# Optimization experiments

Hardware: AMD Instinct MI355X
Metric: run time of the kernel (lower is better)

The kernel has to match this reference:

```python
import jax, jax.numpy as jnp
import numpy as np

NUM_EXPERTS = 4  # matches init_kwargs

def setup_inputs() -> dict:
    key = jax.random.key(0)
    ks = jax.random.split(key, 6)
    B, T, D = 4, 4096, 1024
    H = 4 * D
    x = jax.random.normal(ks[0], (B, T, D), dtype=jnp.float32)
    token_mask = jax.random.randint(ks[1], (B, T), 0, NUM_EXPERTS, dtype=jnp.int32)
    s1 = 1.0 / np.sqrt(D)
    s2 = 1.0 / np.sqrt(H)
    W1 = jax.random.normal(ks[2], (H, D), dtype=jnp.float32) * s1
    b1 = jax.random.normal(ks[3], (H,), dtype=jnp.float32) * s1
    W2 = jax.random.normal(ks[4], (D, H), dtype=jnp.float32) * s2
    b2 = jax.random.normal(ks[5], (D,), dtype=jnp.float32) * s2
    return {"x": x, "token_mask": token_mask, "W1": W1, "b1": b1, "W2": W2, "b2": b2}

def reference(x, token_mask, W1, b1, W2, b2):
    # Nested MoE FFN: expert m uses leading D//2^(E-1-m) input dims and
    # leading H//2^(E-1-m) hidden dims; top expert (m=E-1) is the full MLP.
    D = x.shape[-1]
    H = W1.shape[0]
    factor = 2 ** (NUM_EXPERTS - 1 - token_mask)          # [B,T] int
    d_in = D // factor                                     # [B,T]
    d_hid = H // factor                                    # [B,T]
    mask_in = (jnp.arange(D) < d_in[..., None]).astype(x.dtype)    # [B,T,D]
    mask_hid = (jnp.arange(H) < d_hid[..., None]).astype(x.dtype)  # [B,T,H]
    # Expand: slice input dims, project, keep only nested hidden slice (bias included only there)
    h = (jnp.einsum('btd,hd->bth', x * mask_in, W1) + b1) * mask_hid
    h = jax.nn.gelu(h, approximate=False)  # gelu(0)=0 preserves nested zeros
    # Contract: zeros outside the nested hidden slice contribute nothing; full output + bias
    out = jnp.einsum('bth,dh->btd', h, W2) + b2
    return out
```

## Files before the change

kernel.cpp:

```cpp
#include <hip/hip_runtime.h>
#include <cstdint>
#include <math.h>

typedef __attribute__((ext_vector_type(8))) __bf16 bf16x8;
typedef __attribute__((ext_vector_type(4))) float f32x4;
typedef unsigned short ushort_t;

__device__ __forceinline__ ushort_t f2bf(float f) {
    uint32_t u = __float_as_uint(f);
    u += 0x7fff + ((u >> 16) & 1);
    return (ushort_t)(u >> 16);
}

__device__ __forceinline__ float gelu_fast(float x) {
    float u = x * (0.7978845608f + 0.0356774081f * x * x);
    float e = __expf(2.0f * u);
    float th = 1.0f - 2.0f / (e + 1.0f);
    return 0.5f * x * (1.0f + th);
}

__device__ __forceinline__ float gelu_exact(float v) {
    return 0.5f * v * (1.0f + erff(v * 0.70710678118654752440f));
}

__global__ void histo_convw_kernel(const int* __restrict__ tm, int* __restrict__ cnt,
                                   int nchunks,
                                   const float* __restrict__ s1, const float* __restrict__ s2,
                                   ushort_t* __restrict__ d1, ushort_t* __restrict__ d2,
                                   int n4) {
    if (blockIdx.x < (unsigned)nchunks) {
        __shared__ int h[4];
        if (threadIdx.x < 4) h[threadIdx.x] = 0;
        __syncthreads();
        int e = tm[blockIdx.x * 256 + threadIdx.x];
        atomicAdd(&h[e], 1);
        __syncthreads();
        if (threadIdx.x < 4) cnt[blockIdx.x * 4 + threadIdx.x] = h[threadIdx.x];
    } else {
        const int stride = (gridDim.x - nchunks) * 256;
        for (int i = (blockIdx.x - nchunks) * 256 + threadIdx.x; i < 2 * n4; i += stride) {
            const float* src; ushort_t* dst; int k;
            if (i < n4) { src = s1; dst = d1; k = i; }
            else        { src = s2; dst = d2; k = i - n4; }
            const float4 v = ((const float4*)src)[k];
            ushort4 o;
            o.x = f2bf(v.x); o.y = f2bf(v.y); o.z = f2bf(v.z); o.w = f2bf(v.w);
            ((ushort4*)dst)[k] = o;
        }
    }
}

__global__ void meta_kernel(int* __restrict__ meta, int* __restrict__ cnt,
                            int* __restrict__ sidx, int nchunks, int D, int H) {
    __shared__ int tot[4];
    __shared__ int soff_s[4];
    const int t = threadIdx.x;
    const int e = t >> 6;
    const int c0 = t & 63;
    int carry = 0;
    for (int base = 0; base < nchunks; base += 64) {
        int c = base + c0;
        int v = (c < nchunks) ? cnt[c * 4 + e] : 0;
        int s = v;
#pragma unroll
        for (int d = 1; d < 64; d <<= 1) {
            int y = __shfl_up(s, d);
            if (c0 >= d) s += y;
        }
        if (c < nchunks) cnt[c * 4 + e] = s - v + carry;
        carry += __shfl(s, 63);
    }
    if (c0 == 0) tot[e] = carry;
    __syncthreads();
    if (t == 0) {
        int off = 0, xoff = 0, hoff = 0;
        for (int ee = 0; ee < 4; ee++) {
            int c = tot[ee];
            int ac = (c + 127) & ~127;
            meta[ee] = c; meta[4 + ee] = off; meta[8 + ee] = ac; meta[12 + ee] = ac >> 7;
            meta[16 + ee] = xoff; meta[20 + ee] = hoff;
            soff_s[ee] = off;
            off += ac; xoff += ac * (D >> (3 - ee)); hoff += ac * (H >> (3 - ee));
        }
        meta[28] = off;
        int a = 0, b = 0;
        for (int k = 0; k < 4; k++) {
            int ee = 3 - k;
            meta[24 + k] = a; a += meta[12 + ee] * ((H >> (3 - ee)) >> 7);
            meta[32 + k] = b; b += meta[12 + ee] * (D >> 7);
        }
        meta[29] = a; meta[36] = b;
    }
    __syncthreads();
    for (int base = 0; base < 64 * ((nchunks + 63) / 64); base += 64) {
        int c = base + c0;
        if (c < nchunks) cnt[c * 4 + e] += soff_s[e];
    }
    for (int ee = 0; ee < 4; ee++) {
        int s0 = soff_s[ee] + tot[ee];
        int n = meta[8 + ee] - tot[ee];
        for (int i = t; i < n; i += 256) sidx[s0 + i] = -1;
    }
}

__global__ void place_kernel(const int* __restrict__ tm, const int* __restrict__ cofs,
                             int* __restrict__ sidx) {
    __shared__ unsigned char se[256];
    const int c = blockIdx.x;
    const int t = threadIdx.x;
    const int tok = c * 256 + t;
    const int e = tm[tok];
    se[t] = (unsigned char)e;
    __syncthreads();
    int rank = 0;
    for (int i = 0; i < t; i++) rank += (se[i] == (unsigned char)e);
    sidx[cofs[c * 4 + e] + rank] = tok;
}

__global__ void convert_x_sorted(const float* __restrict__ x,
                                 const int* __restrict__ meta,
                                 const int* __restrict__ sidx,
                                 ushort_t* __restrict__ xb, int D) {
    const int rows = meta[28];
    for (int p = blockIdx.x; p < rows; p += gridDim.x) {
        const int e = (p >= meta[5]) + (p >= meta[6]) + (p >= meta[7]);
        const int off = meta[4 + e];
        const int din = D >> (3 - e);
        const int tok = sidx[p];
        ushort_t* dst = xb + (size_t)meta[16 + e] + (size_t)(p - off) * din;
        const int c = threadIdx.x * 4;
        if (c < din) {
            if (tok < 0) {
                *(ushort4*)(dst + c) = ushort4{0, 0, 0, 0};
            } else {
                const float4 v = *(const float4*)(x + (size_t)tok * D + c);
                ushort4 o;
                o.x = f2bf(v.x); o.y = f2bf(v.y); o.z = f2bf(v.z); o.w = f2bf(v.w);
                *(ushort4*)(dst + c) = o;
            }
        }
    }
}

__device__ __forceinline__ void stage4(const ushort_t* Ag, const ushort_t* Bg,
                                       int lda, int ldb,
                                       char* AsB, char* BsB, int ldsoff) {
    __builtin_amdgcn_global_load_lds(
        (__attribute__((address_space(1))) void*)(uintptr_t)Ag,
        (__attribute__((address_space(3))) void*)(AsB + ldsoff), 16, 0, 0);
    __builtin_amdgcn_global_load_lds(
        (__attribute__((address_space(1))) void*)(uintptr_t)(Ag + (size_t)64 * lda),
        (__attribute__((address_space(3))) void*)(AsB + 4096 + ldsoff), 16, 0, 0);
    __builtin_amdgcn_global_load_lds(
        (__attribute__((address_space(1))) void*)(uintptr_t)Bg,
        (__attribute__((address_space(3))) void*)(BsB + ldsoff), 16, 0, 0);
    __builtin_amdgcn_global_load_lds(
        (__attribute__((address_space(1))) void*)(uintptr_t)(Bg + (size_t)64 * ldb),
        (__attribute__((address_space(3))) void*)(BsB + 4096 + ldsoff), 16, 0, 0);
}

template <int EPI>
__global__ void gemm_sorted(const ushort_t* __restrict__ Abuf,
                            const ushort_t* __restrict__ Bw,
                            const float* __restrict__ bias,
                            const int* __restrict__ meta,
                            const int* __restrict__ sidx,
                            ushort_t* __restrict__ hb,
                            float* __restrict__ out,
                            int D, int H) {
    __shared__ ushort_t As[3][128 * 32];
    __shared__ ushort_t Bs[3][128 * 32];

    const int t    = threadIdx.x;
    const int wave = t >> 6;
    const int lane = t & 63;
    const int quad = lane >> 4;
    const int l16  = lane & 15;
    const int wm   = wave & 1;
    const int wn   = wave >> 1;
    const int srow = t >> 2;
    const int scol = (t & 3) * 8;
    const int ldsoff = wave * 64 * 16;

    const int* st = meta + (EPI == 0 ? 24 : 32);
    const int  T  = meta[EPI == 0 ? 29 : 36];

    for (int idx = blockIdx.x; idx < T; idx += gridDim.x) {
        const int k3 = (idx >= st[1]) + (idx >= st[2]) + (idx >= st[3]);
        const int e = 3 - k3;
        const int local = idx - st[k3];
        const int mtiles = meta[12 + e];
        const int mt = local % mtiles;
        const int nt = local / mtiles;

        const int K   = (EPI == 0) ? (D >> (3 - e)) : (H >> (3 - e));
        const int Ne  = (EPI == 0) ? (H >> (3 - e)) : D;
        const int lda = K;
        const int ldb = (EPI == 0) ? D : H;
        const int nb  = nt * 128;
        const ushort_t* A = Abuf + (size_t)((EPI == 0) ? meta[16 + e] : meta[20 + e]);

        const ushort_t* Ag = A + (size_t)(mt * 128 + srow) * lda + scol;
        const ushort_t* Bg = Bw + (size_t)(nb + srow) * ldb + scol;

        const int nsteps = K >> 5;

        f32x4 acc[4][4] = {};

        stage4(Ag,      Bg,      lda, ldb, (char*)As[0], (char*)Bs[0], ldsoff);
        stage4(Ag + 32, Bg + 32, lda, ldb, (char*)As[1], (char*)Bs[1], ldsoff);
        stage4(Ag + 64, Bg + 64, lda, ldb, (char*)As[2], (char*)Bs[2], ldsoff);

        int cur = 0;
        for (int s = 0; s < nsteps; ++s) {
            const int rem = nsteps - s;
            if (rem > 2)       { asm volatile("s_waitcnt vmcnt(8)" ::: "memory"); }
            else if (rem == 2) { asm volatile("s_waitcnt vmcnt(4)" ::: "memory"); }
            else               { asm volatile("s_waitcnt vmcnt(0)" ::: "memory"); }
            __builtin_amdgcn_s_barrier();
            asm volatile("" ::: "memory");

            bf16x8 af[4], bfr[4];
#pragma unroll
            for (int i = 0; i < 4; i++) {
                af[i]  = *(const bf16x8*)(As[cur] + (wm * 64 + i * 16 + l16) * 32 + quad * 8);
                bfr[i] = *(const bf16x8*)(Bs[cur] + (wn * 64 + i * 16 + l16) * 32 + quad * 8);
            }
            asm volatile("s_waitcnt lgkmcnt(0)" ::: "memory");
            __builtin_amdgcn_s_barrier();
            asm volatile("" ::: "memory");

            if (s + 3 < nsteps)
                stage4(Ag + (size_t)(s + 3) * 32, Bg + (size_t)(s + 3) * 32,
                       lda, ldb, (char*)As[cur], (char*)Bs[cur], ldsoff);

#pragma unroll
            for (int i = 0; i < 4; i++)
#pragma unroll
                for (int j = 0; j < 4; j++)
                    acc[i][j] = __builtin_amdgcn_mfma_f32_16x16x32_bf16(af[i], bfr[j], acc[i][j], 0, 0, 0);

            cur = (cur == 2) ? 0 : cur + 1;
        }

        const int colbase = nb + wn * 64 + l16;
        float bv[4];
#pragma unroll
        for (int j = 0; j < 4; j++) bv[j] = bias[colbase + j * 16];

#pragma unroll
        for (int i = 0; i < 4; i++) {
#pragma unroll
            for (int r = 0; r < 4; r++) {
                const int lrow = mt * 128 + wm * 64 + i * 16 + quad * 4 + r;
                if (EPI == 0) {
                    ushort_t* dst = hb + (size_t)meta[20 + e] + (size_t)lrow * Ne;
#pragma unroll
                    for (int j = 0; j < 4; j++)
                        dst[colbase + j * 16] = f2bf(gelu_fast(acc[i][j][r] + bv[j]));
                } else {
                    const int tok = sidx[meta[4 + e] + lrow];
                    if (tok >= 0) {
                        float* dst = out + (size_t)tok * D;
#pragma unroll
                        for (int j = 0; j < 4; j++)
                            dst[colbase + j * 16] = acc[i][j][r] + bv[j];
                    }
                }
            }
        }
    }
}

__global__ void naive_kernel(const float* __restrict__ x, const int* __restrict__ tm,
                             const float* __restrict__ W1, const float* __restrict__ b1,
                             const float* __restrict__ W2, const float* __restrict__ b2,
                             float* __restrict__ out, int D, int Hdim) {
    const int t = blockIdx.x;
    const int m = tm[t];
    const int din = D >> (3 - m);
    const int dh = Hdim >> (3 - m);
    extern __shared__ float sm[];
    float* xs = sm;
    float* hs = sm + D;
    for (int i = threadIdx.x; i < din; i += blockDim.x) xs[i] = x[(size_t)t * D + i];
    __syncthreads();
    for (int h = threadIdx.x; h < dh; h += blockDim.x) {
        const float* w = W1 + (size_t)h * D;
        float a = b1[h];
        for (int d = 0; d < din; d++) a += xs[d] * w[d];
        hs[h] = gelu_exact(a);
    }
    __syncthreads();
    for (int d = threadIdx.x; d < D; d += blockDim.x) {
        const float* w = W2 + (size_t)d * Hdim;
        float a = b2[d];
        for (int h = 0; h < dh; h++) a += hs[h] * w[h];
        out[(size_t)t * D + d] = a;
    }
}

extern "C" void kernel_launch(void* const* d_in, const int* in_sizes, int n_in,
                              void* d_out, int out_size, void* d_ws, size_t ws_size,
                              hipStream_t stream) {
    const float* x  = (const float*)d_in[0];
    const int* tm   = (const int*)d_in[1];
    const float* W1 = (const float*)d_in[2];
    const float* b1 = (const float*)d_in[3];
    const float* W2 = (const float*)d_in[4];
    const float* b2 = (const float*)d_in[5];
    float* out = (float*)d_out;

    const int M    = in_sizes[1];
    const int Hdim = in_sizes[3];
    const int D    = in_sizes[0] / M;

    const int Mpad = M + 512;
    const int nchunks = M / 256;
    const size_t meta_sz = 256;
    const size_t cnt_sz  = ((size_t)nchunks * 4 * 4 + 255) & ~(size_t)255;
    const size_t sidx_sz = ((size_t)Mpad * 4 + 255) & ~(size_t)255;
    const size_t xb_sz   = (size_t)Mpad * D * 2;
    const size_t w1_sz   = (size_t)Hdim * D * 2;
    const size_t w2_sz   = (size_t)D * Hdim * 2;
    const size_t hb_sz   = (size_t)Mpad * Hdim * 2;
    const size_t need_sorted = meta_sz + cnt_sz + sidx_sz + xb_sz + w1_sz + w2_sz + hb_sz;

    const bool shape_ok = (M % 256 == 0) && (D % 128 == 0) && (Hdim % 128 == 0) &&
                          (D >= 1024) && (D <= 1024) && (Hdim >= 4096);

    if (shape_ok && ws_size >= need_sorted) {
        char* p = (char*)d_ws;
        int* meta     = (int*)p;        p += meta_sz;
        int* cnt      = (int*)p;        p += cnt_sz;
        int* sidx     = (int*)p;        p += sidx_sz;
        ushort_t* xb  = (ushort_t*)p;   p += xb_sz;
        ushort_t* w1b = (ushort_t*)p;   p += w1_sz;
        ushort_t* w2b = (ushort_t*)p;   p += w2_sz;
        ushort_t* hb  = (ushort_t*)p;

        const int n4w = Hdim * D / 4;
        histo_convw_kernel<<<nchunks + 2048, 256, 0, stream>>>(tm, cnt, nchunks,
                                                               W1, W2, w1b, w2b, n4w);
        meta_kernel<<<1, 256, 0, stream>>>(meta, cnt, sidx, nchunks, D, Hdim);
        place_kernel<<<nchunks, 256, 0, stream>>>(tm, cnt, sidx);
        convert_x_sorted<<<2048, 256, 0, stream>>>(x, meta, sidx, xb, D);

        gemm_sorted<0><<<2048, 256, 0, stream>>>(xb, w1b, b1, meta, sidx, hb, nullptr, D, Hdim);
        gemm_sorted<1><<<2048, 256, 0, stream>>>(hb, w2b, b2, meta, sidx, nullptr, out, D, Hdim);
        return;
    }

    const size_t shmem = (size_t)(D + Hdim) * sizeof(float);
    naive_kernel<<<M, 256, shmem, stream>>>(x, tm, W1, b1, W2, b2, out, D, Hdim);
}
```

Before: 330.3 us.

## Use atomic tile scheduler and split-K within block for second GEMM

Both GEMMs now pull tile indices from a global atomic counter rather than using a static grid-stride loop. Launches are sized to a fixed number of persistent blocks. The second GEMM runs 512 threads per block as two 256-thread groups, each handling half of K with its own LDS triple buffer, then reduces through shared memory before the scattered output write. The aim is better load balance across the largest-first expert tiles and more parallelism for the long-K, few-tile second GEMM, at the cost of atomics, extra barriers, a shared-memory reduction and lower occupancy from 96KB of LDS.

```diff
diff --git a/kernel.cpp b/kernel.cpp
--- a/kernel.cpp
+++ b/kernel.cpp
@@ -90,6 +90,8 @@
             meta[32 + k] = b; b += meta[12 + ee] * (D >> 7);
         }
         meta[29] = a; meta[36] = b;
+        meta[48] = 0;
+        meta[49] = 0;
     }
     __syncthreads();
     for (int base = 0; base < 64 * ((nchunks + 63) / 64); base += 64) {
@@ -159,17 +161,16 @@
         (__attribute__((address_space(3))) void*)(BsB + 4096 + ldsoff), 16, 0, 0);
 }
 
-template <int EPI>
-__global__ void gemm_sorted(const ushort_t* __restrict__ Abuf,
-                            const ushort_t* __restrict__ Bw,
-                            const float* __restrict__ bias,
-                            const int* __restrict__ meta,
-                            const int* __restrict__ sidx,
-                            ushort_t* __restrict__ hb,
-                            float* __restrict__ out,
-                            int D, int H) {
+__global__ void gemm1_kernel(const ushort_t* __restrict__ Abuf,
+                             const ushort_t* __restrict__ Bw,
+                             const float* __restrict__ bias,
+                             const int* meta,
+                             ushort_t* __restrict__ hb,
+                             int* tctr,
+                             int D, int H) {
     __shared__ ushort_t As[3][128 * 32];
     __shared__ ushort_t Bs[3][128 * 32];
+    __shared__ int s_next;
 
     const int t    = threadIdx.x;
     const int wave = t >> 6;
@@ -182,10 +183,15 @@
     const int scol = (t & 3) * 8;
     const int ldsoff = wave * 64 * 16;
 
-    const int* st = meta + (EPI == 0 ? 24 : 32);
-    const int  T  = meta[EPI == 0 ? 29 : 36];
-
-    for (int idx = blockIdx.x; idx < T; idx += gridDim.x) {
+    const int* st = meta + 24;
+    const int  T  = meta[29];
+
+    while (true) {
+        if (t == 0) s_next = atomicAdd(tctr, 1);
+        __syncthreads();
+        const int idx = s_next;
+        if (idx >= T) break;
+
         const int k3 = (idx >= st[1]) + (idx >= st[2]) + (idx >= st[3]);
         const int e = 3 - k3;
         const int local = idx - st[k3];
@@ -193,12 +199,12 @@
         const int mt = local % mtiles;
         const int nt = local / mtiles;
 
-        const int K   = (EPI == 0) ? (D >> (3 - e)) : (H >> (3 - e));
-        const int Ne  = (EPI == 0) ? (H >> (3 - e)) : D;
+        const int K   = D >> (3 - e);
+        const int Ne  = H >> (3 - e);
         const int lda = K;
-        const int ldb = (EPI == 0) ? D : H;
+        const int ldb = D;
         const int nb  = nt * 128;
-        const ushort_t* A = Abuf + (size_t)((EPI == 0) ? meta[16 + e] : meta[20 + e]);
+        const ushort_t* A = Abuf + (size_t)meta[16 + e];
 
         const ushort_t* Ag = A + (size_t)(mt * 128 + srow) * lda + scol;
         const ushort_t* Bg = Bw + (size_t)(nb + srow) * ldb + scol;
@@ -253,22 +259,153 @@
 #pragma unroll
             for (int r = 0; r < 4; r++) {
                 const int lrow = mt * 128 + wm * 64 + i * 16 + quad * 4 + r;
-                if (EPI == 0) {
-                    ushort_t* dst = hb + (size_t)meta[20 + e] + (size_t)lrow * Ne;
+                ushort_t* dst = hb + (size_t)meta[20 + e] + (size_t)lrow * Ne;
+#pragma unroll
+                for (int j = 0; j < 4; j++)
+                    dst[colbase + j * 16] = f2bf(gelu_fast(acc[i][j][r] + bv[j]));
+            }
+        }
+        __syncthreads();
+    }
+}
+
+__global__ __launch_bounds__(512)
+void gemm2_kernel(const ushort_t* __restrict__ Abuf,
+                  const ushort_t* __restrict__ Bw,
+                  const float* __restrict__ bias,
+                  const int* meta,
+                  const int* __restrict__ sidx,
+                  float* __restrict__ out,
+                  int* tctr,
+                  int D, int H) {
+    __shared__ char smem[98304];
+    __shared__ int s_next;
+
+    const int t    = threadIdx.x;
+    const int g    = t >> 8;
+    const int tl   = t & 255;
+    const int wiv  = tl >> 6;
+    const int lane = t & 63;
+    const int quad = lane >> 4;
+    const int l16  = lane & 15;
+    const int wm   = wiv & 1;
+    const int wn   = wiv >> 1;
+    const int srow = tl >> 2;
+    const int scol = (tl & 3) * 8;
+    const int ldsoff = wiv * 64 * 16;
+
+    const int* st = meta + 32;
+    const int  T  = meta[36];
+
+    while (true) {
+        if (t == 0) s_next = atomicAdd(tctr, 1);
+        __syncthreads();
+        const int idx = s_next;
+        if (idx >= T) break;
+
+        const int k3 = (idx >= st[1]) + (idx >= st[2]) + (idx >= st[3]);
+        const int e = 3 - k3;
+        const int local = idx - st[k3];
+        const int mtiles = meta[12 + e];
+        const int mt = local % mtiles;
+        const int nt = local / mtiles;
+
+        const int Kfull = H >> (3 - e);
+        const int Kh    = Kfull >> 1;
+        const int lda = Kfull;
+        const int ldb = H;
+        const int nb  = nt * 128;
+        const ushort_t* A = Abuf + (size_t)meta[20 + e];
+
+        const ushort_t* Ag = A + (size_t)(mt * 128 + srow) * lda + scol + (size_t)g * Kh;
+        const ushort_t* Bg = Bw + (size_t)(nb + srow) * ldb + scol + (size_t)g * Kh;
+
+        const int nsteps = Kh >> 5;
+
+        char* buf0 = smem + (size_t)(g * 3 + 0) * 16384;
+        char* buf1 = smem + (size_t)(g * 3 + 1) * 16384;
+        char* buf2 = smem + (size_t)(g * 3 + 2) * 16384;
+
+        f32x4 acc[4][4] = {};
+
+        stage4(Ag,      Bg,      lda, ldb, buf0, buf0 + 8192, ldsoff);
+        stage4(Ag + 32, Bg + 32, lda, ldb, buf1, buf1 + 8192, ldsoff);
+        stage4(Ag + 64, Bg + 64, lda, ldb, buf2, buf2 + 8192, ldsoff);
+
+        int cur = 0;
+        for (int s = 0; s < nsteps; ++s) {
+            const int rem = nsteps - s;
+            if (rem > 2)       { asm volatile("s_waitcnt vmcnt(8)" ::: "memory"); }
+            else if (rem == 2) { asm volatile("s_waitcnt vmcnt(4)" ::: "memory"); }
+            else               { asm volatile("s_waitcnt vmcnt(0)" ::: "memory"); }
+            __builtin_amdgcn_s_barrier();
+            asm volatile("" ::: "memory");
+
+            char* bc = smem + (size_t)(g * 3 + cur) * 16384;
+            const ushort_t* Asc = (const ushort_t*)bc;
+            const ushort_t* Bsc = (const ushort_t*)(bc + 8192);
+
+            bf16x8 af[4], bfr[4];
+#pragma unroll
+            for (int i = 0; i < 4; i++) {
+                af[i]  = *(const bf16x8*)(Asc + (wm * 64 + i * 16 + l16) * 32 + quad * 8);
+                bfr[i] = *(const bf16x8*)(Bsc + (wn * 64 + i * 16 + l16) * 32 + quad * 8);
+            }
+            asm volatile("s_waitcnt lgkmcnt(0)" ::: "memory");
+            __builtin_amdgcn_s_barrier();
+            asm volatile("" ::: "memory");
+
+            if (s + 3 < nsteps)
+                stage4(Ag + (size_t)(s + 3) * 32, Bg + (size_t)(s + 3) * 32,
+                       lda, ldb, bc, bc + 8192, ldsoff);
+
+#pragma unroll
+            for (int i = 0; i < 4; i++)
+#pragma unroll
+                for (int j = 0; j < 4; j++)
+                    acc[i][j] = __builtin_amdgcn_mfma_f32_16x16x32_bf16(af[i], bfr[j], acc[i][j], 0, 0, 0);
+
+            cur = (cur == 2) ? 0 : cur + 1;
+        }
+
+        float* red = (float*)smem;
+        __syncthreads();
+        if (g == 1) {
+#pragma unroll
+            for (int i = 0; i < 4; i++)
+#pragma unroll
+                for (int r = 0; r < 4; r++) {
+                    const int lrl = wm * 64 + i * 16 + quad * 4 + r;
 #pragma unroll
                     for (int j = 0; j < 4; j++)
-                        dst[colbase + j * 16] = f2bf(gelu_fast(acc[i][j][r] + bv[j]));
-                } else {
+                        red[lrl * 128 + wn * 64 + j * 16 + l16] = acc[i][j][r];
+                }
+        }
+        __syncthreads();
+        if (g == 0) {
+            const int colbase = nb + wn * 64 + l16;
+            float bv[4];
+#pragma unroll
+            for (int j = 0; j < 4; j++) bv[j] = bias[colbase + j * 16];
+
+#pragma unroll
+            for (int i = 0; i < 4; i++) {
+#pragma unroll
+                for (int r = 0; r < 4; r++) {
+                    const int lrl  = wm * 64 + i * 16 + quad * 4 + r;
+                    const int lrow = mt * 128 + lrl;
                     const int tok = sidx[meta[4 + e] + lrow];
                     if (tok >= 0) {
                         float* dst = out + (size_t)tok * D;
 #pragma unroll
                         for (int j = 0; j < 4; j++)
-                            dst[colbase + j * 16] = acc[i][j][r] + bv[j];
+                            dst[colbase + j * 16] =
+                                acc[i][j][r] + red[lrl * 128 + wn * 64 + j * 16 + l16] + bv[j];
                     }
                 }
             }
         }
+        __syncthreads();
     }
 }
 
@@ -346,8 +483,8 @@
         place_kernel<<<nchunks, 256, 0, stream>>>(tm, cnt, sidx);
         convert_x_sorted<<<2048, 256, 0, stream>>>(x, meta, sidx, xb, D);
 
-        gemm_sorted<0><<<2048, 256, 0, stream>>>(xb, w1b, b1, meta, sidx, hb, nullptr, D, Hdim);
-        gemm_sorted<1><<<2048, 256, 0, stream>>>(hb, w2b, b2, meta, sidx, nullptr, out, D, Hdim);
+        gemm1_kernel<<<768, 256, 0, stream>>>(xb, w1b, b1, meta, hb, meta + 48, D, Hdim);
+        gemm2_kernel<<<256, 512, 0, stream>>>(hb, w2b, b2, meta, sidx, out, meta + 49, D, Hdim);
         return;
     }
 
```

Result: slower. 384.1 us (+16.3%).

## Assign GEMM tiles per XCD for L2 locality and use ballot-based ranking in place

Applied to the files above, without the earlier changes.

Tile scheduling for both GEMMs is rebuilt so that blocks on each of the 8 XCDs (taken as blockIdx & 7) own a contiguous slice of N tiles (first GEMM) or M tiles (second GEMM). Per-XCD prefix tables are precomputed in meta, which grows to 1 KB. The goal is more weight/activation reuse within each XCD's private L2. Separately, place_kernel replaces its O(256) serial shared-memory rank loop with wave ballots and popcounts. The risk is load imbalance across XCDs, and the loop stride of 256 assumes a fixed grid of 2048 blocks.

```diff
diff --git a/kernel.cpp b/kernel.cpp
--- a/kernel.cpp
+++ b/kernel.cpp
@@ -83,13 +83,25 @@
             off += ac; xoff += ac * (D >> (3 - ee)); hoff += ac * (H >> (3 - ee));
         }
         meta[28] = off;
-        int a = 0, b = 0;
-        for (int k = 0; k < 4; k++) {
-            int ee = 3 - k;
-            meta[24 + k] = a; a += meta[12 + ee] * ((H >> (3 - ee)) >> 7);
-            meta[32 + k] = b; b += meta[12 + ee] * (D >> 7);
-        }
-        meta[29] = a; meta[36] = b;
+        const int nt2 = D >> 7;
+        for (int x = 0; x < 8; x++) {
+            int s1 = 0, s2 = 0;
+            for (int k = 0; k < 4; k++) {
+                int ee = 3 - k;
+                int mtl = meta[12 + ee];
+                meta[64 + x * 8 + k] = s1;
+                int q = ((H >> (3 - ee)) >> 7) >> 3;
+                int c1 = q ? (mtl * q)
+                           : ((x & 1) ? (mtl - (mtl >> 1)) : (mtl >> 1));
+                s1 += c1;
+                meta[128 + x * 8 + k] = s2;
+                int qm = mtl >> 3, rm = mtl & 7;
+                int cm = qm + ((x < rm) ? 1 : 0);
+                s2 += cm * nt2;
+            }
+            meta[64 + x * 8 + 4] = s1;
+            meta[128 + x * 8 + 4] = s2;
+        }
     }
     __syncthreads();
     for (int base = 0; base < 64 * ((nchunks + 63) / 64); base += 64) {
@@ -105,15 +117,24 @@
 
 __global__ void place_kernel(const int* __restrict__ tm, const int* __restrict__ cofs,
                              int* __restrict__ sidx) {
-    __shared__ unsigned char se[256];
+    __shared__ int wc[4][4];
     const int c = blockIdx.x;
     const int t = threadIdx.x;
+    const int wave = t >> 6;
+    const int lane = t & 63;
     const int tok = c * 256 + t;
     const int e = tm[tok];
-    se[t] = (unsigned char)e;
-    __syncthreads();
-    int rank = 0;
-    for (int i = 0; i < t; i++) rank += (se[i] == (unsigned char)e);
+    unsigned long long bal[4];
+#pragma unroll
+    for (int v = 0; v < 4; v++) bal[v] = __ballot(e == v);
+    if (lane < 4) wc[wave][lane] = __popcll(bal[lane]);
+    __syncthreads();
+    int pre = 0;
+#pragma unroll
+    for (int w = 0; w < 4; w++)
+        if (w < wave) pre += wc[w][e];
+    const unsigned long long lower = (1ull << lane) - 1ull;
+    const int rank = pre + __popcll(bal[e] & lower);
     sidx[cofs[c * 4 + e] + rank] = tok;
 }
 
@@ -182,16 +203,31 @@
     const int scol = (t & 3) * 8;
     const int ldsoff = wave * 64 * 16;
 
-    const int* st = meta + (EPI == 0 ? 24 : 32);
-    const int  T  = meta[EPI == 0 ? 29 : 36];
-
-    for (int idx = blockIdx.x; idx < T; idx += gridDim.x) {
-        const int k3 = (idx >= st[1]) + (idx >= st[2]) + (idx >= st[3]);
+    const int xcd   = blockIdx.x & 7;
+    const int rank0 = blockIdx.x >> 3;
+    const int* xst  = meta + (EPI == 0 ? 64 : 128) + xcd * 8;
+    const int  Tx   = xst[4];
+
+    for (int r = rank0; r < Tx; r += 256) {
+        const int k3 = (r >= xst[1]) + (r >= xst[2]) + (r >= xst[3]);
         const int e = 3 - k3;
-        const int local = idx - st[k3];
+        const int rl = r - xst[k3];
         const int mtiles = meta[12 + e];
-        const int mt = local % mtiles;
-        const int nt = local / mtiles;
+
+        int mt, nt;
+        if (EPI == 0) {
+            const int q = ((H >> (3 - e)) >> 7) >> 3;
+            if (q) { mt = rl / q; nt = xcd * q + (rl - mt * q); }
+            else   { const int m0 = mtiles >> 1;
+                     nt = xcd >> 1;
+                     mt = (xcd & 1) ? (m0 + rl) : rl; }
+        } else {
+            const int qm = mtiles >> 3, rm = mtiles & 7;
+            const int cm = qm + ((xcd < rm) ? 1 : 0);
+            const int bm = xcd * qm + ((xcd < rm) ? xcd : rm);
+            nt = rl / cm;
+            mt = bm + (rl - nt * cm);
+        }
 
         const int K   = (EPI == 0) ? (D >> (3 - e)) : (H >> (3 - e));
         const int Ne  = (EPI == 0) ? (H >> (3 - e)) : D;
@@ -251,20 +287,20 @@
 #pragma unroll
         for (int i = 0; i < 4; i++) {
 #pragma unroll
-            for (int r = 0; r < 4; r++) {
-                const int lrow = mt * 128 + wm * 64 + i * 16 + quad * 4 + r;
+            for (int r2 = 0; r2 < 4; r2++) {
+                const int lrow = mt * 128 + wm * 64 + i * 16 + quad * 4 + r2;
                 if (EPI == 0) {
                     ushort_t* dst = hb + (size_t)meta[20 + e] + (size_t)lrow * Ne;
 #pragma unroll
                     for (int j = 0; j < 4; j++)
-                        dst[colbase + j * 16] = f2bf(gelu_fast(acc[i][j][r] + bv[j]));
+                        dst[colbase + j * 16] = f2bf(gelu_fast(acc[i][j][r2] + bv[j]));
                 } else {
                     const int tok = sidx[meta[4 + e] + lrow];
                     if (tok >= 0) {
                         float* dst = out + (size_t)tok * D;
 #pragma unroll
                         for (int j = 0; j < 4; j++)
-                            dst[colbase + j * 16] = acc[i][j][r] + bv[j];
+                            dst[colbase + j * 16] = acc[i][j][r2] + bv[j];
                     }
                 }
             }
@@ -317,7 +353,7 @@
 
     const int Mpad = M + 512;
     const int nchunks = M / 256;
-    const size_t meta_sz = 256;
+    const size_t meta_sz = 1024;
     const size_t cnt_sz  = ((size_t)nchunks * 4 * 4 + 255) & ~(size_t)255;
     const size_t sidx_sz = ((size_t)Mpad * 4 + 255) & ~(size_t)255;
     const size_t xb_sz   = (size_t)Mpad * D * 2;
```

Result: faster. 314.9 us (-4.7%).
